# Kernel optimization log

Hardware: AMD Instinct MI355X
Metric: run time of the kernel (lower is better)

## Reference

```python
import jax, jax.numpy as jnp
import numpy as np
from jax import lax

V, H, A, S = 256, 2048, 512, 512  # vocab, hidden, attn, seq_len


def setup_inputs() -> dict:
    key = jax.random.key(0)
    ks = jax.random.split(key, 8)
    sc = 0.02  # small init to keep tanh unsaturated
    return {
        "x_enc": jax.random.normal(ks[0], (S, V), jnp.float32),
        "x_dec": jax.random.normal(ks[1], (S, V), jnp.float32),
        "W_enc": jax.random.normal(ks[2], (H, V + H), jnp.float32) * sc,
        "b_enc": jnp.zeros((H,), jnp.float32),
        "Wa_enc": jax.random.normal(ks[3], (A, H), jnp.float32) * sc,
        "Wa_dec": jax.random.normal(ks[4], (A, H), jnp.float32) * sc,
        "v_a": jax.random.normal(ks[5], (A,), jnp.float32) * sc,
        "W_dec": jax.random.normal(ks[6], (H, V + 2 * H), jnp.float32) * sc,
        "b_dec": jnp.zeros((H,), jnp.float32),
        "W_out": jax.random.normal(ks[7], (V, H), jnp.float32) * sc,
        "b_out": jnp.zeros((V,), jnp.float32),
    }


def reference(x_enc, x_dec, W_enc, b_enc, Wa_enc, Wa_dec, v_a, W_dec, b_dec, W_out, b_out):
    h0 = jnp.zeros((W_enc.shape[0],), x_enc.dtype)

    # Encoder: h_t = tanh(W_enc [x_t ; h_{t-1}] + b)
    def enc_step(h, x):
        h_new = jnp.tanh(jnp.concatenate([x, h]) @ W_enc.T + b_enc)
        return h_new, h_new

    h_enc, enc_states = lax.scan(enc_step, h0, x_enc)  # enc_states: (S, H)

    # Encoder-side attention projection is step-invariant -> hoist (same math).
    enc_proj = enc_states @ Wa_enc.T  # (S, A)

    # Decoder with per-step Bahdanau additive attention.
    def dec_step(h, x):
        dec_proj = h @ Wa_dec.T                              # (A,)
        energy = jnp.tanh(enc_proj + dec_proj) @ v_a         # (S,)
        attn_w = jax.nn.softmax(energy)                      # (S,)
        context = attn_w @ enc_states                        # (H,)
        h_new = jnp.tanh(jnp.concatenate([x, context, h]) @ W_dec.T + b_dec)
        logits = h_new @ W_out.T + b_out                     # (V,)
        return h_new, logits

    _, outputs = lax.scan(dec_step, h_enc, x_dec)  # (S, V)
    return outputs
```

## Files before the change

### kernel.cpp

```cpp
#include <hip/hip_runtime.h>

#define V 256
#define H 2048
#define A 512
#define S 512
#define NBLK 128
#define NTHR 512
#define CH 64
#define HPH (512*CH)
#define DPH (128*CH)
#define SENTU 0x7FC00000u

typedef float f32x4 __attribute__((ext_vector_type(4)));
typedef float f32x2 __attribute__((ext_vector_type(2)));

__device__ __forceinline__ f32x4 ld_cg4(const float* p) {
    f32x4 r;
    asm volatile("global_load_dwordx4 %0, %1, off sc0 sc1\n\ts_waitcnt vmcnt(0)"
                 : "=&v"(r) : "v"(p) : "memory");
    return r;
}
__device__ __forceinline__ f32x4 poll4(const float* p) {
    f32x4 r = ld_cg4(p);
    while (__float_as_uint(r.x) == SENTU || __float_as_uint(r.y) == SENTU ||
           __float_as_uint(r.z) == SENTU || __float_as_uint(r.w) == SENTU)
        r = ld_cg4(p);
    return r;
}
__device__ __forceinline__ void st_pub2(float* p, float x, float y) {
    f32x2 v; v.x = x; v.y = y;
    asm volatile("s_waitcnt vmcnt(0)\n\tglobal_store_dwordx2 %0, %1, off sc0 sc1"
                 :: "v"(p), "v"(v) : "memory");
}
__device__ __forceinline__ void st_pub1(float* p, float x) {
    asm volatile("s_waitcnt vmcnt(0)\n\tglobal_store_dword %0, %1, off sc0 sc1"
                 :: "v"(p), "v"(x) : "memory");
}
__device__ __forceinline__ void st_rst2(float* p) {
    f32x2 v; v.x = __uint_as_float(SENTU); v.y = __uint_as_float(SENTU);
    asm volatile("global_store_dwordx2 %0, %1, off sc0 sc1" :: "v"(p), "v"(v) : "memory");
}
__device__ __forceinline__ void st_rst1(float* p) {
    float v = __uint_as_float(SENTU);
    asm volatile("global_store_dword %0, %1, off sc0 sc1" :: "v"(p), "v"(v) : "memory");
}

__global__ void init_ex(unsigned* p, int n) {
    int i = blockIdx.x * blockDim.x + threadIdx.x;
    if (i < n) p[i] = SENTU;
}

__global__ __launch_bounds__(256) void gemm_nt(
    const float* __restrict__ Amat, int lda,
    const float* __restrict__ Bmat, int ldb,
    float* __restrict__ C, int ldc,
    const float* __restrict__ bias, int M, int N, int K)
{
    __shared__ float As[16][68];
    __shared__ float Bs[16][68];
    const int tid = threadIdx.x;
    const int tx = tid & 15;
    const int ty = tid >> 4;
    const int m0 = blockIdx.y * 64;
    const int n0 = blockIdx.x * 64;
    const int lr = tid >> 2;
    const int lk = (tid & 3) * 4;

    float acc[4][4] = {};
    for (int k0 = 0; k0 < K; k0 += 16) {
        float4 av = *(const float4*)(Amat + (size_t)(m0 + lr) * lda + k0 + lk);
        float4 bv = *(const float4*)(Bmat + (size_t)(n0 + lr) * ldb + k0 + lk);
        __syncthreads();
        As[lk+0][lr] = av.x; As[lk+1][lr] = av.y; As[lk+2][lr] = av.z; As[lk+3][lr] = av.w;
        Bs[lk+0][lr] = bv.x; Bs[lk+1][lr] = bv.y; Bs[lk+2][lr] = bv.z; Bs[lk+3][lr] = bv.w;
        __syncthreads();
        #pragma unroll
        for (int k = 0; k < 16; ++k) {
            float a4[4], b4[4];
            #pragma unroll
            for (int i = 0; i < 4; ++i) a4[i] = As[k][ty*4+i];
            #pragma unroll
            for (int j = 0; j < 4; ++j) b4[j] = Bs[k][tx*4+j];
            #pragma unroll
            for (int i = 0; i < 4; ++i)
                #pragma unroll
                for (int j = 0; j < 4; ++j) acc[i][j] += a4[i] * b4[j];
        }
    }
    #pragma unroll
    for (int i = 0; i < 4; ++i) {
        const int m = m0 + ty*4 + i;
        #pragma unroll
        for (int j = 0; j < 4; ++j) {
            const int n = n0 + tx*4 + j;
            float v = acc[i][j];
            if (bias) v += bias[n];
            C[(size_t)m * ldc + n] = v;
        }
    }
}

__global__ __launch_bounds__(NTHR, 2) void enc_scan(
    const float* __restrict__ W_enc, const float* __restrict__ accx,
    float* __restrict__ states, float* __restrict__ hex)
{
    __shared__ __align__(16) float hs[2][H];
    const int tid = threadIdx.x;
    const int wid = tid >> 6, lane = tid & 63;
    const int w   = blockIdx.x * 8 + wid;
    const int r0  = 2*w, r1 = r0 + 1;
    const int slot = (w >> 1)*CH + (w & 1)*2;

    f32x4 we0[8], we1[8];
    #pragma unroll
    for (int k = 0; k < 8; ++k) {
        we0[k] = *(const f32x4*)(W_enc + (size_t)r0*(V+H) + V + 4*(lane + 64*k));
        we1[k] = *(const f32x4*)(W_enc + (size_t)r1*(V+H) + V + 4*(lane + 64*k));
    }

    if (lane == 0) {
        float h0 = tanhf(accx[r0]), h1 = tanhf(accx[r1]);
        states[r0] = h0; states[r1] = h1;
        st_pub2(hex + slot, h0, h1);
    }

    for (int t = 1; t < S; ++t) {
        float ax0 = 0.f, ax1 = 0.f;
        if (lane == 0) { ax0 = accx[(size_t)t*H + r0]; ax1 = accx[(size_t)t*H + r1]; }

        f32x4 c = poll4(hex + ((t-1)%3)*HPH + tid*CH);
        ((f32x4*)hs[t&1])[tid] = c;
        __syncthreads();

        if (lane == 0) st_rst2(hex + ((t+1)%3)*HPH + slot);

        const f32x4* h4 = (const f32x4*)hs[t&1];
        float a0 = 0.f, a1 = 0.f;
        #pragma unroll
        for (int k = 0; k < 8; ++k) {
            f32x4 hv = h4[lane + 64*k];
            a0 += we0[k].x*hv.x + we0[k].y*hv.y + we0[k].z*hv.z + we0[k].w*hv.w;
            a1 += we1[k].x*hv.x + we1[k].y*hv.y + we1[k].z*hv.z + we1[k].w*hv.w;
        }
        #pragma unroll
        for (int off = 32; off; off >>= 1) { a0 += __shfl_down(a0, off); a1 += __shfl_down(a1, off); }
        if (lane == 0) {
            float h0 = tanhf(a0 + ax0);
            float h1 = tanhf(a1 + ax1);
            states[(size_t)t*H + r0] = h0; states[(size_t)t*H + r1] = h1;
            st_pub2(hex + (t%3)*HPH + slot, h0, h1);
        }
    }
}

__global__ __launch_bounds__(NTHR, 2) void dec_scan(
    const float* __restrict__ Wa_dec, const float* __restrict__ W_dec,
    const float* __restrict__ enc_proj, const float* __restrict__ v_a,
    const float* __restrict__ WcT, const float* __restrict__ accx,
    const float* __restrict__ enc_states, float* __restrict__ h_dec,
    float* __restrict__ hexd, float* __restrict__ dpex, float* __restrict__ eex)
{
    __shared__ __align__(16) float hs[H];
    __shared__ __align__(16) float ps[A];
    __shared__ __align__(16) float es[S];
    __shared__ float zred[8];
    const int tid = threadIdx.x;
    const int wid = tid >> 6, lane = tid & 63;
    const int w   = blockIdx.x * 8 + wid;
    const int r0  = 2*w, r1 = r0 + 1;
    const int hslot = (w >> 1)*CH + (w & 1)*2;
    const bool attn = ((w & 1) == 0);
    const int s_row = w >> 1;
    const int aslot = (s_row >> 2)*CH + (s_row & 3);

    f32x4 wh0[8], wh1[8], wa[8], wc0[2], wc1[2], ep[2], va[2];
    #pragma unroll
    for (int k = 0; k < 8; ++k) {
        wh0[k] = *(const f32x4*)(W_dec + (size_t)r0*(V+2*H) + V + H + 4*(lane + 64*k));
        wh1[k] = *(const f32x4*)(W_dec + (size_t)r1*(V+2*H) + V + H + 4*(lane + 64*k));
        wa[k]  = (f32x4)(0.f);
    }
    #pragma unroll
    for (int k = 0; k < 2; ++k) {
        wc0[k] = *(const f32x4*)(WcT + (size_t)r0*S + 4*(lane + 64*k));
        wc1[k] = *(const f32x4*)(WcT + (size_t)r1*S + 4*(lane + 64*k));
        ep[k] = (f32x4)(0.f); va[k] = (f32x4)(0.f);
    }
    if (attn) {
        #pragma unroll
        for (int k = 0; k < 8; ++k)
            wa[k] = *(const f32x4*)(Wa_dec + (size_t)s_row*H + 4*(lane + 64*k));
        #pragma unroll
        for (int k = 0; k < 2; ++k) {
            ep[k] = *(const f32x4*)(enc_proj + (size_t)s_row*A + 4*(lane + 64*k));
            va[k] = *(const f32x4*)(v_a + 4*(lane + 64*k));
        }
    }
    const f32x4* hs4 = (const f32x4*)hs;
    const f32x4* ps4 = (const f32x4*)ps;
    const f32x4* es4 = (const f32x4*)es;

    for (int t = 0; t < S; ++t) {
        float ax0 = 0.f, ax1 = 0.f;
        if (lane == 0) { ax0 = accx[(size_t)t*H + r0]; ax1 = accx[(size_t)t*H + r1]; }

        if (t == 0) {
            ((f32x4*)hs)[tid] = ((const f32x4*)(enc_states + (size_t)(S-1)*H))[tid];
        } else {
            f32x4 c = poll4(hexd + ((t-1)%3)*HPH + tid*CH);
            ((f32x4*)hs)[tid] = c;
        }
        __syncthreads();

        if (t > 0 && lane == 0) {
            st_rst2(hexd + ((t+1)%3)*HPH + hslot);
            if (attn) {
                st_rst1(dpex + ((t-1)%3)*DPH + aslot);
                st_rst1(eex  + ((t-1)%3)*DPH + aslot);
            }
        }

        if (attn) {
            float aP = 0.f;
            #pragma unroll
            for (int k = 0; k < 8; ++k) {
                f32x4 hv = hs4[lane + 64*k];
                aP += wa[k].x*hv.x + wa[k].y*hv.y + wa[k].z*hv.z + wa[k].w*hv.w;
            }
            #pragma unroll
            for (int off = 32; off; off >>= 1) aP += __shfl_down(aP, off);
            if (lane == 0) st_pub1(dpex + (t%3)*DPH + aslot, aP);
        }
        float aH0 = 0.f, aH1 = 0.f;
        #pragma unroll
        for (int k = 0; k < 8; ++k) {
            f32x4 hv = hs4[lane + 64*k];
            aH0 += wh0[k].x*hv.x + wh0[k].y*hv.y + wh0[k].z*hv.z + wh0[k].w*hv.w;
            aH1 += wh1[k].x*hv.x + wh1[k].y*hv.y + wh1[k].z*hv.z + wh1[k].w*hv.w;
        }
        #pragma unroll
        for (int off = 32; off; off >>= 1) { aH0 += __shfl_down(aH0, off); aH1 += __shfl_down(aH1, off); }

        if (tid < 128) {
            f32x4 c = poll4(dpex + (t%3)*DPH + tid*CH);
            ((f32x4*)ps)[tid] = c;
        }
        __syncthreads();
        if (attn) {
            float e_ = 0.f;
            #pragma unroll
            for (int k = 0; k < 2; ++k) {
                f32x4 p = ps4[lane + 64*k];
                e_ += va[k].x*tanhf(ep[k].x + p.x) + va[k].y*tanhf(ep[k].y + p.y)
                    + va[k].z*tanhf(ep[k].z + p.z) + va[k].w*tanhf(ep[k].w + p.w);
            }
            #pragma unroll
            for (int off = 32; off; off >>= 1) e_ += __shfl_down(e_, off);
            if (lane == 0) st_pub1(eex + (t%3)*DPH + aslot, expf(e_));
        }

        if (tid < 128) {
            f32x4 c = poll4(eex + (t%3)*DPH + tid*CH);
            ((f32x4*)es)[tid] = c;
        }
        __syncthreads();

        float z = es[tid];
        #pragma unroll
        for (int off = 32; off; off >>= 1) z += __shfl_down(z, off);
        if (lane == 0) zred[wid] = z;
        __syncthreads();
        const float Z = zred[0]+zred[1]+zred[2]+zred[3]+zred[4]+zred[5]+zred[6]+zred[7];

        float c0 = 0.f, c1 = 0.f;
        #pragma unroll
        for (int k = 0; k < 2; ++k) {
            f32x4 ev = es4[lane + 64*k];
            c0 += wc0[k].x*ev.x + wc0[k].y*ev.y + wc0[k].z*ev.z + wc0[k].w*ev.w;
            c1 += wc1[k].x*ev.x + wc1[k].y*ev.y + wc1[k].z*ev.z + wc1[k].w*ev.w;
        }
        #pragma unroll
        for (int off = 32; off; off >>= 1) { c0 += __shfl_down(c0, off); c1 += __shfl_down(c1, off); }
        if (lane == 0) {
            const float Zi = 1.f / Z;
            float h0 = tanhf(ax0 + aH0 + c0*Zi);
            float h1 = tanhf(ax1 + aH1 + c1*Zi);
            h_dec[(size_t)t*H + r0] = h0; h_dec[(size_t)t*H + r1] = h1;
            st_pub2(hexd + (t%3)*HPH + hslot, h0, h1);
        }
    }
}

extern "C" void kernel_launch(void* const* d_in, const int* in_sizes, int n_in,
                              void* d_out, int out_size, void* d_ws, size_t ws_size,
                              hipStream_t stream) {
    const float* x_enc  = (const float*)d_in[0];
    const float* x_dec  = (const float*)d_in[1];
    const float* W_enc  = (const float*)d_in[2];
    const float* b_enc  = (const float*)d_in[3];
    const float* Wa_enc = (const float*)d_in[4];
    const float* Wa_dec = (const float*)d_in[5];
    const float* v_a    = (const float*)d_in[6];
    const float* W_dec  = (const float*)d_in[7];
    const float* b_dec  = (const float*)d_in[8];
    const float* W_out  = (const float*)d_in[9];
    const float* b_out  = (const float*)d_in[10];
    float* out = (float*)d_out;

    float* ws         = (float*)d_ws;
    float* accx_enc   = ws;
    float* enc_states = accx_enc + (size_t)S*H;
    float* enc_proj   = enc_states + (size_t)S*H;
    float* WcT        = enc_proj + (size_t)S*A;
    float* accx_dec   = WcT + (size_t)H*S;
    float* h_dec      = accx_dec + (size_t)S*H;
    float* hex_e      = h_dec + (size_t)S*H;
    float* hex_d      = hex_e + 3*HPH;
    float* dp_ex      = hex_d + 3*HPH;
    float* e_ex       = dp_ex + 3*DPH;
    const int n_ex = 3*HPH*2 + 3*DPH*2;

    dim3 b256(256);

    init_ex<<<dim3((n_ex + 255)/256), b256, 0, stream>>>((unsigned*)hex_e, n_ex);

    gemm_nt<<<dim3(H/64, S/64), b256, 0, stream>>>(x_enc, V, W_enc, V+H, accx_enc, H, b_enc, S, H, V);
    gemm_nt<<<dim3(H/64, S/64), b256, 0, stream>>>(x_dec, V, W_dec, V+2*H, accx_dec, H, b_dec, S, H, V);

    {
        const float* We = W_enc; const float* ax = accx_enc; float* st = enc_states; float* hx = hex_e;
        void* args[] = { &We, &ax, &st, &hx };
        hipLaunchCooperativeKernel((void*)enc_scan, dim3(NBLK), dim3(NTHR), args, 0, stream);
    }

    gemm_nt<<<dim3(A/64, S/64), b256, 0, stream>>>(enc_states, H, Wa_enc, H, enc_proj, A, nullptr, S, A, H);
    gemm_nt<<<dim3(S/64, H/64), b256, 0, stream>>>(W_dec + V, V+2*H, enc_states, H, WcT, S, nullptr, H, S, H);

    {
        const float* wa = Wa_dec; const float* wd = W_dec; const float* epj = enc_proj;
        const float* vv = v_a; const float* wc = WcT; const float* ax = accx_dec;
        const float* est = enc_states; float* hd = h_dec;
        float* hx = hex_d; float* dx = dp_ex; float* ex = e_ex;
        void* args[] = { &wa, &wd, &epj, &vv, &wc, &ax, &est, &hd, &hx, &dx, &ex };
        hipLaunchCooperativeKernel((void*)dec_scan, dim3(NBLK), dim3(NTHR), args, 0, stream);
    }

    gemm_nt<<<dim3(V/64, S/64), b256, 0, stream>>>(h_dec, H, W_out, H, out, V, b_out, S, V, H);
}
```

Baseline: 6.185 ms.

## Replace packed vector-load polling with per-producer atomic slots

Cross-block exchange buffers are re-laid out so that each producing wave owns its own 256-byte slot. Values are published and polled with device-scope relaxed atomic exchange and fetch_add instead of sc0/sc1 vector loads and stores into shared 16-byte groups. This is meant to cut false sharing and repeated polling of cache lines that several producers write. The cost is more poll operations per thread (two 64-bit polls for h, one poll per thread for attention values instead of 128 threads) and atomics that travel to L2.

```diff
diff --git a/kernel.cpp b/kernel.cpp
--- a/kernel.cpp
+++ b/kernel.cpp
@@ -7,42 +7,32 @@
 #define NBLK 128
 #define NTHR 512
 #define CH 64
-#define HPH (512*CH)
-#define DPH (128*CH)
+#define HPH (1024*CH)
+#define DPH (512*CH)
 #define SENTU 0x7FC00000u
+#define SENT64 0x7FC000007FC00000ULL
 
 typedef float f32x4 __attribute__((ext_vector_type(4)));
-typedef float f32x2 __attribute__((ext_vector_type(2)));
-
-__device__ __forceinline__ f32x4 ld_cg4(const float* p) {
-    f32x4 r;
-    asm volatile("global_load_dwordx4 %0, %1, off sc0 sc1\n\ts_waitcnt vmcnt(0)"
-                 : "=&v"(r) : "v"(p) : "memory");
-    return r;
-}
-__device__ __forceinline__ f32x4 poll4(const float* p) {
-    f32x4 r = ld_cg4(p);
-    while (__float_as_uint(r.x) == SENTU || __float_as_uint(r.y) == SENTU ||
-           __float_as_uint(r.z) == SENTU || __float_as_uint(r.w) == SENTU)
-        r = ld_cg4(p);
-    return r;
-}
-__device__ __forceinline__ void st_pub2(float* p, float x, float y) {
-    f32x2 v; v.x = x; v.y = y;
-    asm volatile("s_waitcnt vmcnt(0)\n\tglobal_store_dwordx2 %0, %1, off sc0 sc1"
-                 :: "v"(p), "v"(v) : "memory");
-}
-__device__ __forceinline__ void st_pub1(float* p, float x) {
-    asm volatile("s_waitcnt vmcnt(0)\n\tglobal_store_dword %0, %1, off sc0 sc1"
-                 :: "v"(p), "v"(x) : "memory");
-}
-__device__ __forceinline__ void st_rst2(float* p) {
-    f32x2 v; v.x = __uint_as_float(SENTU); v.y = __uint_as_float(SENTU);
-    asm volatile("global_store_dwordx2 %0, %1, off sc0 sc1" :: "v"(p), "v"(v) : "memory");
-}
-__device__ __forceinline__ void st_rst1(float* p) {
-    float v = __uint_as_float(SENTU);
-    asm volatile("global_store_dword %0, %1, off sc0 sc1" :: "v"(p), "v"(v) : "memory");
+typedef unsigned long long u64;
+
+__device__ __forceinline__ void vm_drain() { asm volatile("s_waitcnt vmcnt(0)" ::: "memory"); }
+__device__ __forceinline__ u64 ax_poll64(u64* p) {
+    return __hip_atomic_fetch_add(p, 0ULL, __ATOMIC_RELAXED, __HIP_MEMORY_SCOPE_AGENT);
+}
+__device__ __forceinline__ unsigned ax_poll32(unsigned* p) {
+    return __hip_atomic_fetch_add(p, 0u, __ATOMIC_RELAXED, __HIP_MEMORY_SCOPE_AGENT);
+}
+__device__ __forceinline__ void ax_st64(u64* p, u64 v) {
+    (void)__hip_atomic_exchange(p, v, __ATOMIC_RELAXED, __HIP_MEMORY_SCOPE_AGENT);
+}
+__device__ __forceinline__ void ax_st32(unsigned* p, unsigned v) {
+    (void)__hip_atomic_exchange(p, v, __ATOMIC_RELAXED, __HIP_MEMORY_SCOPE_AGENT);
+}
+__device__ __forceinline__ bool bad64(u64 v) {
+    return ((unsigned)v == SENTU) || ((unsigned)(v >> 32) == SENTU);
+}
+__device__ __forceinline__ u64 pack2(float a, float b) {
+    return ((u64)__float_as_uint(b) << 32) | (u64)__float_as_uint(a);
 }
 
 __global__ void init_ex(unsigned* p, int n) {
@@ -109,7 +99,6 @@
     const int wid = tid >> 6, lane = tid & 63;
     const int w   = blockIdx.x * 8 + wid;
     const int r0  = 2*w, r1 = r0 + 1;
-    const int slot = (w >> 1)*CH + (w & 1)*2;
 
     f32x4 we0[8], we1[8];
     #pragma unroll
@@ -121,18 +110,30 @@
     if (lane == 0) {
         float h0 = tanhf(accx[r0]), h1 = tanhf(accx[r1]);
         states[r0] = h0; states[r1] = h1;
-        st_pub2(hex + slot, h0, h1);
+        vm_drain();
+        ax_st64((u64*)(hex + 0*HPH + w*CH), pack2(h0, h1));
     }
 
     for (int t = 1; t < S; ++t) {
         float ax0 = 0.f, ax1 = 0.f;
         if (lane == 0) { ax0 = accx[(size_t)t*H + r0]; ax1 = accx[(size_t)t*H + r1]; }
 
-        f32x4 c = poll4(hex + ((t-1)%3)*HPH + tid*CH);
-        ((f32x4*)hs[t&1])[tid] = c;
-        __syncthreads();
-
-        if (lane == 0) st_rst2(hex + ((t+1)%3)*HPH + slot);
+        {
+            float* hb = hex + ((t-1)%3)*HPH;
+            u64* s0 = (u64*)(hb + tid*CH);
+            u64* s1 = (u64*)(hb + (tid+512)*CH);
+            u64 a = ax_poll64(s0), b = ax_poll64(s1);
+            while (bad64(a)) a = ax_poll64(s0);
+            while (bad64(b)) b = ax_poll64(s1);
+            float* dst = hs[t&1];
+            dst[2*tid]        = __uint_as_float((unsigned)a);
+            dst[2*tid+1]      = __uint_as_float((unsigned)(a >> 32));
+            dst[1024+2*tid]   = __uint_as_float((unsigned)b);
+            dst[1024+2*tid+1] = __uint_as_float((unsigned)(b >> 32));
+        }
+        __syncthreads();
+
+        if (lane == 0) ax_st64((u64*)(hex + ((t+1)%3)*HPH + w*CH), SENT64);
 
         const f32x4* h4 = (const f32x4*)hs[t&1];
         float a0 = 0.f, a1 = 0.f;
@@ -148,7 +149,8 @@
             float h0 = tanhf(a0 + ax0);
             float h1 = tanhf(a1 + ax1);
             states[(size_t)t*H + r0] = h0; states[(size_t)t*H + r1] = h1;
-            st_pub2(hex + (t%3)*HPH + slot, h0, h1);
+            vm_drain();
+            ax_st64((u64*)(hex + (t%3)*HPH + w*CH), pack2(h0, h1));
         }
     }
 }
@@ -168,10 +170,8 @@
     const int wid = tid >> 6, lane = tid & 63;
     const int w   = blockIdx.x * 8 + wid;
     const int r0  = 2*w, r1 = r0 + 1;
-    const int hslot = (w >> 1)*CH + (w & 1)*2;
     const bool attn = ((w & 1) == 0);
     const int s_row = w >> 1;
-    const int aslot = (s_row >> 2)*CH + (s_row & 3);
 
     f32x4 wh0[8], wh1[8], wa[8], wc0[2], wc1[2], ep[2], va[2];
     #pragma unroll
@@ -207,16 +207,24 @@
         if (t == 0) {
             ((f32x4*)hs)[tid] = ((const f32x4*)(enc_states + (size_t)(S-1)*H))[tid];
         } else {
-            f32x4 c = poll4(hexd + ((t-1)%3)*HPH + tid*CH);
-            ((f32x4*)hs)[tid] = c;
+            float* hb = hexd + ((t-1)%3)*HPH;
+            u64* s0 = (u64*)(hb + tid*CH);
+            u64* s1 = (u64*)(hb + (tid+512)*CH);
+            u64 a = ax_poll64(s0), b = ax_poll64(s1);
+            while (bad64(a)) a = ax_poll64(s0);
+            while (bad64(b)) b = ax_poll64(s1);
+            hs[2*tid]        = __uint_as_float((unsigned)a);
+            hs[2*tid+1]      = __uint_as_float((unsigned)(a >> 32));
+            hs[1024+2*tid]   = __uint_as_float((unsigned)b);
+            hs[1024+2*tid+1] = __uint_as_float((unsigned)(b >> 32));
         }
         __syncthreads();
 
         if (t > 0 && lane == 0) {
-            st_rst2(hexd + ((t+1)%3)*HPH + hslot);
+            ax_st64((u64*)(hexd + ((t+1)%3)*HPH + w*CH), SENT64);
             if (attn) {
-                st_rst1(dpex + ((t-1)%3)*DPH + aslot);
-                st_rst1(eex  + ((t-1)%3)*DPH + aslot);
+                ax_st32((unsigned*)(dpex + ((t-1)%3)*DPH + s_row*CH), SENTU);
+                ax_st32((unsigned*)(eex  + ((t-1)%3)*DPH + s_row*CH), SENTU);
             }
         }
 
@@ -229,7 +237,10 @@
             }
             #pragma unroll
             for (int off = 32; off; off >>= 1) aP += __shfl_down(aP, off);
-            if (lane == 0) st_pub1(dpex + (t%3)*DPH + aslot, aP);
+            if (lane == 0) {
+                vm_drain();
+                ax_st32((unsigned*)(dpex + (t%3)*DPH + s_row*CH), __float_as_uint(aP));
+            }
         }
         float aH0 = 0.f, aH1 = 0.f;
         #pragma unroll
@@ -241,9 +252,11 @@
         #pragma unroll
         for (int off = 32; off; off >>= 1) { aH0 += __shfl_down(aH0, off); aH1 += __shfl_down(aH1, off); }
 
-        if (tid < 128) {
-            f32x4 c = poll4(dpex + (t%3)*DPH + tid*CH);
-            ((f32x4*)ps)[tid] = c;
+        {
+            unsigned* sp = (unsigned*)(dpex + (t%3)*DPH + tid*CH);
+            unsigned v = ax_poll32(sp);
+            while (v == SENTU) v = ax_poll32(sp);
+            ps[tid] = __uint_as_float(v);
         }
         __syncthreads();
         if (attn) {
@@ -256,12 +269,17 @@
             }
             #pragma unroll
             for (int off = 32; off; off >>= 1) e_ += __shfl_down(e_, off);
-            if (lane == 0) st_pub1(eex + (t%3)*DPH + aslot, expf(e_));
-        }
-
-        if (tid < 128) {
-            f32x4 c = poll4(eex + (t%3)*DPH + tid*CH);
-            ((f32x4*)es)[tid] = c;
+            if (lane == 0) {
+                vm_drain();
+                ax_st32((unsigned*)(eex + (t%3)*DPH + s_row*CH), __float_as_uint(expf(e_)));
+            }
+        }
+
+        {
+            unsigned* sp = (unsigned*)(eex + (t%3)*DPH + tid*CH);
+            unsigned v = ax_poll32(sp);
+            while (v == SENTU) v = ax_poll32(sp);
+            es[tid] = __uint_as_float(v);
         }
         __syncthreads();
 
@@ -286,7 +304,8 @@
             float h0 = tanhf(ax0 + aH0 + c0*Zi);
             float h1 = tanhf(ax1 + aH1 + c1*Zi);
             h_dec[(size_t)t*H + r0] = h0; h_dec[(size_t)t*H + r1] = h1;
-            st_pub2(hexd + (t%3)*HPH + hslot, h0, h1);
+            vm_drain();
+            ax_st64((u64*)(hexd + (t%3)*HPH + w*CH), pack2(h0, h1));
         }
     }
 }
```

Measured after the change: 6.156 ms. About the same (-0.5%).

## Compute next-step decoder attention projection via atomic scatter, cutting one grid exchange

Applied to the files above, without the earlier changes.

In the decoder scan, each block now computes its partial contribution to the next step's Wa_dec·h projection from the h values it just produced. It accumulates these into a global buffer with float atomics and signals completion through a counter. A separate kernel computes the step-0 projection. This removes one full cross-block publish/poll round (the dp exchange) from each step's critical path, and the encoder and decoder now publish via atomic exchanges while resetting sentinels in the same step. The cost is many global float atomics per step, a counter spin-wait, a different floating-point summation order, and occupancy lowered to one block per CU.

```diff
diff --git a/kernel.cpp b/kernel.cpp
--- a/kernel.cpp
+++ b/kernel.cpp
@@ -7,12 +7,16 @@
 #define NBLK 128
 #define NTHR 512
 #define CH 64
+#define CH2 16
 #define HPH (512*CH)
-#define DPH (128*CH)
+#define EPH (128*CH)
+#define DPH (512*CH2)
 #define SENTU 0x7FC00000u
+#define SENT64 0x7FC000007FC00000ULL
 
 typedef float f32x4 __attribute__((ext_vector_type(4)));
 typedef float f32x2 __attribute__((ext_vector_type(2)));
+typedef unsigned long long u64;
 
 __device__ __forceinline__ f32x4 ld_cg4(const float* p) {
     f32x4 r;
@@ -27,27 +31,54 @@
         r = ld_cg4(p);
     return r;
 }
-__device__ __forceinline__ void st_pub2(float* p, float x, float y) {
-    f32x2 v; v.x = x; v.y = y;
-    asm volatile("s_waitcnt vmcnt(0)\n\tglobal_store_dwordx2 %0, %1, off sc0 sc1"
-                 :: "v"(p), "v"(v) : "memory");
-}
-__device__ __forceinline__ void st_pub1(float* p, float x) {
-    asm volatile("s_waitcnt vmcnt(0)\n\tglobal_store_dword %0, %1, off sc0 sc1"
-                 :: "v"(p), "v"(x) : "memory");
-}
-__device__ __forceinline__ void st_rst2(float* p) {
-    f32x2 v; v.x = __uint_as_float(SENTU); v.y = __uint_as_float(SENTU);
-    asm volatile("global_store_dwordx2 %0, %1, off sc0 sc1" :: "v"(p), "v"(v) : "memory");
-}
-__device__ __forceinline__ void st_rst1(float* p) {
-    float v = __uint_as_float(SENTU);
-    asm volatile("global_store_dword %0, %1, off sc0 sc1" :: "v"(p), "v"(v) : "memory");
-}
-
-__global__ void init_ex(unsigned* p, int n) {
+__device__ __forceinline__ unsigned ld_cg1u(const unsigned* p) {
+    unsigned r;
+    asm volatile("global_load_dword %0, %1, off sc0 sc1\n\ts_waitcnt vmcnt(0)"
+                 : "=&v"(r) : "v"(p) : "memory");
+    return r;
+}
+__device__ __forceinline__ void ld_cg8(const float* p0, const float* p1, const float* p2, const float* p3,
+                                       const float* p4, const float* p5, const float* p6, const float* p7,
+                                       float o[8]) {
+    float a0,a1,a2,a3,a4,a5,a6,a7;
+    asm volatile(
+        "global_load_dword %0, %8, off sc0 sc1\n\t"
+        "global_load_dword %1, %9, off sc0 sc1\n\t"
+        "global_load_dword %2, %10, off sc0 sc1\n\t"
+        "global_load_dword %3, %11, off sc0 sc1\n\t"
+        "global_load_dword %4, %12, off sc0 sc1\n\t"
+        "global_load_dword %5, %13, off sc0 sc1\n\t"
+        "global_load_dword %6, %14, off sc0 sc1\n\t"
+        "global_load_dword %7, %15, off sc0 sc1\n\t"
+        "s_waitcnt vmcnt(0)"
+        : "=&v"(a0),"=&v"(a1),"=&v"(a2),"=&v"(a3),"=&v"(a4),"=&v"(a5),"=&v"(a6),"=&v"(a7)
+        : "v"(p0),"v"(p1),"v"(p2),"v"(p3),"v"(p4),"v"(p5),"v"(p6),"v"(p7)
+        : "memory");
+    o[0]=a0;o[1]=a1;o[2]=a2;o[3]=a3;o[4]=a4;o[5]=a5;o[6]=a6;o[7]=a7;
+}
+
+__device__ __forceinline__ void vm_drain() { asm volatile("s_waitcnt vmcnt(0)" ::: "memory"); }
+__device__ __forceinline__ void ax_st64(u64* p, u64 v) {
+    (void)__hip_atomic_exchange(p, v, __ATOMIC_RELAXED, __HIP_MEMORY_SCOPE_AGENT);
+}
+__device__ __forceinline__ void ax_st32(unsigned* p, unsigned v) {
+    (void)__hip_atomic_exchange(p, v, __ATOMIC_RELAXED, __HIP_MEMORY_SCOPE_AGENT);
+}
+__device__ __forceinline__ float ga_addf(float* p, float v) {
+    return __hip_atomic_fetch_add(p, v, __ATOMIC_RELAXED, __HIP_MEMORY_SCOPE_AGENT);
+}
+__device__ __forceinline__ unsigned ga_addu(unsigned* p, unsigned v) {
+    return __hip_atomic_fetch_add(p, v, __ATOMIC_RELAXED, __HIP_MEMORY_SCOPE_AGENT);
+}
+__device__ __forceinline__ u64 pack2(float a, float b) {
+    return ((u64)__float_as_uint(b) << 32) | (u64)__float_as_uint(a);
+}
+
+__global__ void init_ex(unsigned* sent, int n_sent, unsigned* zero, int n_zero, unsigned* cnt) {
     int i = blockIdx.x * blockDim.x + threadIdx.x;
-    if (i < n) p[i] = SENTU;
+    if (i < n_sent) sent[i] = SENTU;
+    if (i < n_zero) zero[i] = 0u;
+    if (i == 0) { cnt[0] = NBLK; cnt[64] = 0u; cnt[128] = 0u; }
 }
 
 __global__ __launch_bounds__(256) void gemm_nt(
@@ -100,11 +131,30 @@
     }
 }
 
+__global__ __launch_bounds__(512) void dp0_kernel(
+    const float* __restrict__ Wa_dec, const float* __restrict__ hN, float* __restrict__ dpacc)
+{
+    const int wid = threadIdx.x >> 6, lane = threadIdx.x & 63;
+    const int a   = blockIdx.x * 8 + wid;
+    const f32x4* w4 = (const f32x4*)(Wa_dec + (size_t)a * H);
+    const f32x4* h4 = (const f32x4*)hN;
+    float acc = 0.f;
+    #pragma unroll
+    for (int k = 0; k < 8; ++k) {
+        f32x4 w = w4[lane + 64*k];
+        f32x4 h = h4[lane + 64*k];
+        acc += w.x*h.x + w.y*h.y + w.z*h.z + w.w*h.w;
+    }
+    #pragma unroll
+    for (int off = 32; off; off >>= 1) acc += __shfl_down(acc, off);
+    if (lane == 0) ax_st32((unsigned*)(dpacc + (size_t)a*CH2), __float_as_uint(acc));
+}
+
 __global__ __launch_bounds__(NTHR, 2) void enc_scan(
     const float* __restrict__ W_enc, const float* __restrict__ accx,
     float* __restrict__ states, float* __restrict__ hex)
 {
-    __shared__ __align__(16) float hs[2][H];
+    __shared__ __align__(16) float hs[H];
     const int tid = threadIdx.x;
     const int wid = tid >> 6, lane = tid & 63;
     const int w   = blockIdx.x * 8 + wid;
@@ -120,21 +170,18 @@
 
     if (lane == 0) {
         float h0 = tanhf(accx[r0]), h1 = tanhf(accx[r1]);
+        vm_drain();
+        ax_st64((u64*)(hex + 0*HPH + slot), pack2(h0, h1));
         states[r0] = h0; states[r1] = h1;
-        st_pub2(hex + slot, h0, h1);
     }
 
     for (int t = 1; t < S; ++t) {
-        float ax0 = 0.f, ax1 = 0.f;
-        if (lane == 0) { ax0 = accx[(size_t)t*H + r0]; ax1 = accx[(size_t)t*H + r1]; }
-
-        f32x4 c = poll4(hex + ((t-1)%3)*HPH + tid*CH);
-        ((f32x4*)hs[t&1])[tid] = c;
-        __syncthreads();
-
-        if (lane == 0) st_rst2(hex + ((t+1)%3)*HPH + slot);
-
-        const f32x4* h4 = (const f32x4*)hs[t&1];
+        float ax0 = accx[(size_t)t*H + r0];
+        float ax1 = accx[(size_t)t*H + r1];
+        ((f32x4*)hs)[tid] = poll4(hex + ((t-1)%3)*HPH + tid*CH);
+        __syncthreads();
+
+        const f32x4* h4 = (const f32x4*)hs;
         float a0 = 0.f, a1 = 0.f;
         #pragma unroll
         for (int k = 0; k < 8; ++k) {
@@ -147,90 +194,93 @@
         if (lane == 0) {
             float h0 = tanhf(a0 + ax0);
             float h1 = tanhf(a1 + ax1);
+            vm_drain();
+            ax_st64((u64*)(hex + (t%3)*HPH + slot), pack2(h0, h1));
             states[(size_t)t*H + r0] = h0; states[(size_t)t*H + r1] = h1;
-            st_pub2(hex + (t%3)*HPH + slot, h0, h1);
-        }
-    }
-}
-
-__global__ __launch_bounds__(NTHR, 2) void dec_scan(
+            ax_st64((u64*)(hex + ((t+1)%3)*HPH + slot), SENT64);
+        }
+    }
+}
+
+__global__ __launch_bounds__(NTHR, 1) void dec_scan(
     const float* __restrict__ Wa_dec, const float* __restrict__ W_dec,
     const float* __restrict__ enc_proj, const float* __restrict__ v_a,
     const float* __restrict__ WcT, const float* __restrict__ accx,
     const float* __restrict__ enc_states, float* __restrict__ h_dec,
-    float* __restrict__ hexd, float* __restrict__ dpex, float* __restrict__ eex)
+    float* __restrict__ hexd, float* __restrict__ eex,
+    float* __restrict__ dpacc, unsigned* __restrict__ cnt)
 {
     __shared__ __align__(16) float hs[H];
-    __shared__ __align__(16) float ps[A];
     __shared__ __align__(16) float es[S];
+    __shared__ float dpl[A];
     __shared__ float zred[8];
     const int tid = threadIdx.x;
     const int wid = tid >> 6, lane = tid & 63;
-    const int w   = blockIdx.x * 8 + wid;
+    const int bid = blockIdx.x;
+    const int w   = bid * 8 + wid;
     const int r0  = 2*w, r1 = r0 + 1;
     const int hslot = (w >> 1)*CH + (w & 1)*2;
     const bool attn = ((w & 1) == 0);
     const int s_row = w >> 1;
-    const int aslot = (s_row >> 2)*CH + (s_row & 3);
-
-    f32x4 wh0[8], wh1[8], wa[8], wc0[2], wc1[2], ep[2], va[2];
+
+    f32x4 wh0[8], wh1[8], wc0[2], wc1[2];
+    float ep_r[8], va_r[8], wac0[8], wac1[8];
     #pragma unroll
     for (int k = 0; k < 8; ++k) {
         wh0[k] = *(const f32x4*)(W_dec + (size_t)r0*(V+2*H) + V + H + 4*(lane + 64*k));
         wh1[k] = *(const f32x4*)(W_dec + (size_t)r1*(V+2*H) + V + H + 4*(lane + 64*k));
-        wa[k]  = (f32x4)(0.f);
+        wac0[k] = Wa_dec[(size_t)(lane + 64*k)*H + r0];
+        wac1[k] = Wa_dec[(size_t)(lane + 64*k)*H + r1];
+        ep_r[k] = 0.f; va_r[k] = 0.f;
     }
     #pragma unroll
     for (int k = 0; k < 2; ++k) {
         wc0[k] = *(const f32x4*)(WcT + (size_t)r0*S + 4*(lane + 64*k));
         wc1[k] = *(const f32x4*)(WcT + (size_t)r1*S + 4*(lane + 64*k));
-        ep[k] = (f32x4)(0.f); va[k] = (f32x4)(0.f);
     }
     if (attn) {
         #pragma unroll
-        for (int k = 0; k < 8; ++k)
-            wa[k] = *(const f32x4*)(Wa_dec + (size_t)s_row*H + 4*(lane + 64*k));
-        #pragma unroll
-        for (int k = 0; k < 2; ++k) {
-            ep[k] = *(const f32x4*)(enc_proj + (size_t)s_row*A + 4*(lane + 64*k));
-            va[k] = *(const f32x4*)(v_a + 4*(lane + 64*k));
+        for (int k = 0; k < 8; ++k) {
+            ep_r[k] = enc_proj[(size_t)s_row*A + lane + 64*k];
+            va_r[k] = v_a[lane + 64*k];
         }
     }
     const f32x4* hs4 = (const f32x4*)hs;
-    const f32x4* ps4 = (const f32x4*)ps;
     const f32x4* es4 = (const f32x4*)es;
 
     for (int t = 0; t < S; ++t) {
-        float ax0 = 0.f, ax1 = 0.f;
-        if (lane == 0) { ax0 = accx[(size_t)t*H + r0]; ax1 = accx[(size_t)t*H + r1]; }
-
-        if (t == 0) {
-            ((f32x4*)hs)[tid] = ((const f32x4*)(enc_states + (size_t)(S-1)*H))[tid];
-        } else {
-            f32x4 c = poll4(hexd + ((t-1)%3)*HPH + tid*CH);
-            ((f32x4*)hs)[tid] = c;
-        }
-        __syncthreads();
-
-        if (t > 0 && lane == 0) {
-            st_rst2(hexd + ((t+1)%3)*HPH + hslot);
-            if (attn) {
-                st_rst1(dpex + ((t-1)%3)*DPH + aslot);
-                st_rst1(eex  + ((t-1)%3)*DPH + aslot);
-            }
-        }
+        const int ph  = t % 3;
+        const int phn = (t+1) % 3;
+        const int php = (t+2) % 3;
+
+        if (t == 0) ((f32x4*)hs)[tid] = ((const f32x4*)(enc_states + (size_t)(S-1)*H))[tid];
+        else        ((f32x4*)hs)[tid] = poll4(hexd + php*HPH + tid*CH);
+        __syncthreads();
 
         if (attn) {
-            float aP = 0.f;
-            #pragma unroll
-            for (int k = 0; k < 8; ++k) {
-                f32x4 hv = hs4[lane + 64*k];
-                aP += wa[k].x*hv.x + wa[k].y*hv.y + wa[k].z*hv.z + wa[k].w*hv.w;
-            }
-            #pragma unroll
-            for (int off = 32; off; off >>= 1) aP += __shfl_down(aP, off);
-            if (lane == 0) st_pub1(dpex + (t%3)*DPH + aslot, aP);
-        }
+            float* dpb = dpacc + ph*DPH;
+            const float* q0 = dpb + (size_t)(lane      )*CH2;
+            const float* q1 = dpb + (size_t)(lane +  64)*CH2;
+            const float* q2 = dpb + (size_t)(lane + 128)*CH2;
+            const float* q3 = dpb + (size_t)(lane + 192)*CH2;
+            const float* q4 = dpb + (size_t)(lane + 256)*CH2;
+            const float* q5 = dpb + (size_t)(lane + 320)*CH2;
+            const float* q6 = dpb + (size_t)(lane + 384)*CH2;
+            const float* q7 = dpb + (size_t)(lane + 448)*CH2;
+            const unsigned* cp = cnt + ph*64;
+            while (ld_cg1u(cp) < NBLK) {}
+            float dpv[8];
+            ld_cg8(q0,q1,q2,q3,q4,q5,q6,q7, dpv);
+            float e_ = 0.f;
+            #pragma unroll
+            for (int k = 0; k < 8; ++k) e_ += va_r[k] * tanhf(ep_r[k] + dpv[k]);
+            #pragma unroll
+            for (int off = 32; off; off >>= 1) e_ += __shfl_xor(e_, off);
+            if (lane == 0)
+                ax_st32((unsigned*)(eex + ph*EPH + (s_row>>2)*CH + (s_row&3)),
+                        __float_as_uint(expf(e_)));
+        }
+
         float aH0 = 0.f, aH1 = 0.f;
         #pragma unroll
         for (int k = 0; k < 8; ++k) {
@@ -239,35 +289,14 @@
             aH1 += wh1[k].x*hv.x + wh1[k].y*hv.y + wh1[k].z*hv.z + wh1[k].w*hv.w;
         }
         #pragma unroll
-        for (int off = 32; off; off >>= 1) { aH0 += __shfl_down(aH0, off); aH1 += __shfl_down(aH1, off); }
-
-        if (tid < 128) {
-            f32x4 c = poll4(dpex + (t%3)*DPH + tid*CH);
-            ((f32x4*)ps)[tid] = c;
-        }
-        __syncthreads();
-        if (attn) {
-            float e_ = 0.f;
-            #pragma unroll
-            for (int k = 0; k < 2; ++k) {
-                f32x4 p = ps4[lane + 64*k];
-                e_ += va[k].x*tanhf(ep[k].x + p.x) + va[k].y*tanhf(ep[k].y + p.y)
-                    + va[k].z*tanhf(ep[k].z + p.z) + va[k].w*tanhf(ep[k].w + p.w);
-            }
-            #pragma unroll
-            for (int off = 32; off; off >>= 1) e_ += __shfl_down(e_, off);
-            if (lane == 0) st_pub1(eex + (t%3)*DPH + aslot, expf(e_));
-        }
-
-        if (tid < 128) {
-            f32x4 c = poll4(eex + (t%3)*DPH + tid*CH);
-            ((f32x4*)es)[tid] = c;
-        }
+        for (int off = 32; off; off >>= 1) { aH0 += __shfl_xor(aH0, off); aH1 += __shfl_xor(aH1, off); }
+
+        if (tid < 128) ((f32x4*)es)[tid] = poll4(eex + ph*EPH + tid*CH);
         __syncthreads();
 
         float z = es[tid];
         #pragma unroll
-        for (int off = 32; off; off >>= 1) z += __shfl_down(z, off);
+        for (int off = 32; off; off >>= 1) z += __shfl_xor(z, off);
         if (lane == 0) zred[wid] = z;
         __syncthreads();
         const float Z = zred[0]+zred[1]+zred[2]+zred[3]+zred[4]+zred[5]+zred[6]+zred[7];
@@ -280,14 +309,38 @@
             c1 += wc1[k].x*ev.x + wc1[k].y*ev.y + wc1[k].z*ev.z + wc1[k].w*ev.w;
         }
         #pragma unroll
-        for (int off = 32; off; off >>= 1) { c0 += __shfl_down(c0, off); c1 += __shfl_down(c1, off); }
+        for (int off = 32; off; off >>= 1) { c0 += __shfl_xor(c0, off); c1 += __shfl_xor(c1, off); }
+
+        const float Zi = 1.f / Z;
+        const float ax0 = accx[(size_t)t*H + r0];
+        const float ax1 = accx[(size_t)t*H + r1];
+        const float h0 = tanhf(ax0 + aH0 + c0*Zi);
+        const float h1 = tanhf(ax1 + aH1 + c1*Zi);
         if (lane == 0) {
-            const float Zi = 1.f / Z;
-            float h0 = tanhf(ax0 + aH0 + c0*Zi);
-            float h1 = tanhf(ax1 + aH1 + c1*Zi);
-            h_dec[(size_t)t*H + r0] = h0; h_dec[(size_t)t*H + r1] = h1;
-            st_pub2(hexd + (t%3)*HPH + hslot, h0, h1);
-        }
+            vm_drain();
+            ax_st64((u64*)(hexd + ph*HPH + hslot), pack2(h0, h1));
+            f32x2 hv; hv.x = h0; hv.y = h1;
+            *(f32x2*)(h_dec + (size_t)t*H + r0) = hv;
+        }
+
+        if (t < S-1) {
+            dpl[tid] = 0.f;
+            __syncthreads();
+            #pragma unroll
+            for (int k = 0; k < 8; ++k)
+                atomicAdd(&dpl[lane + 64*k], wac0[k]*h0 + wac1[k]*h1);
+            __syncthreads();
+            (void)ga_addf(dpacc + phn*DPH + (size_t)tid*CH2, dpl[tid]);
+            vm_drain();
+            __syncthreads();
+            if (tid == 0) (void)ga_addu(cnt + phn*64, 1u);
+        }
+
+        if (lane == 0) ax_st64((u64*)(hexd + phn*HPH + hslot), SENT64);
+        if (t > 0 && attn && lane == 0)
+            ax_st32((unsigned*)(eex + php*EPH + (s_row>>2)*CH + (s_row&3)), SENTU);
+        if (tid < 4) ax_st32((unsigned*)(dpacc + ph*DPH + (size_t)(4*bid+tid)*CH2), 0u);
+        if (bid == 0 && tid == 0) ax_st32(cnt + ph*64, 0u);
     }
 }
 
@@ -316,13 +369,16 @@
     float* h_dec      = accx_dec + (size_t)S*H;
     float* hex_e      = h_dec + (size_t)S*H;
     float* hex_d      = hex_e + 3*HPH;
-    float* dp_ex      = hex_d + 3*HPH;
-    float* e_ex       = dp_ex + 3*DPH;
-    const int n_ex = 3*HPH*2 + 3*DPH*2;
+    float* e_ex       = hex_d + 3*HPH;
+    float* dpacc      = e_ex + 3*EPH;
+    unsigned* cnt     = (unsigned*)(dpacc + 3*DPH);
+    const int n_sent = 3*HPH*2 + 3*EPH;
+    const int n_zero = 3*DPH;
 
     dim3 b256(256);
 
-    init_ex<<<dim3((n_ex + 255)/256), b256, 0, stream>>>((unsigned*)hex_e, n_ex);
+    init_ex<<<dim3((n_sent + 255)/256), b256, 0, stream>>>(
+        (unsigned*)hex_e, n_sent, (unsigned*)dpacc, n_zero, cnt);
 
     gemm_nt<<<dim3(H/64, S/64), b256, 0, stream>>>(x_enc, V, W_enc, V+H, accx_enc, H, b_enc, S, H, V);
     gemm_nt<<<dim3(H/64, S/64), b256, 0, stream>>>(x_dec, V, W_dec, V+2*H, accx_dec, H, b_dec, S, H, V);
@@ -335,13 +391,16 @@
 
     gemm_nt<<<dim3(A/64, S/64), b256, 0, stream>>>(enc_states, H, Wa_enc, H, enc_proj, A, nullptr, S, A, H);
     gemm_nt<<<dim3(S/64, H/64), b256, 0, stream>>>(W_dec + V, V+2*H, enc_states, H, WcT, S, nullptr, H, S, H);
+    {
+        dp0_kernel<<<dim3(64), dim3(512), 0, stream>>>(Wa_dec, enc_states + (size_t)(S-1)*H, dpacc);
+    }
 
     {
         const float* wa = Wa_dec; const float* wd = W_dec; const float* epj = enc_proj;
         const float* vv = v_a; const float* wc = WcT; const float* ax = accx_dec;
         const float* est = enc_states; float* hd = h_dec;
-        float* hx = hex_d; float* dx = dp_ex; float* ex = e_ex;
-        void* args[] = { &wa, &wd, &epj, &vv, &wc, &ax, &est, &hd, &hx, &dx, &ex };
+        float* hx = hex_d; float* ex = e_ex; float* dpa = dpacc; unsigned* cc = cnt;
+        void* args[] = { &wa, &wd, &epj, &vv, &wc, &ax, &est, &hd, &hx, &ex, &dpa, &cc };
         hipLaunchCooperativeKernel((void*)dec_scan, dim3(NBLK), dim3(NTHR), args, 0, stream);
     }
 
```

Result: slower. 10.35 ms (+67.3%).

## Aggregate per-block hidden-state publishes into 64-byte chunks for cross-block exchange

Applied to the files above, without the earlier changes.

Each block now gathers its 16 hidden outputs in shared memory and one thread publishes them as a single 64-byte chunk per block, instead of each wave publishing a 2-float slot into a padded 64-float line. Readers poll 128 chunks with four 16-byte loads each rather than 512 padded slots, which shrinks the exchange buffer and the number of coherent global transactions per step. The cost is an extra __syncthreads before each publish, and a single publisher thread per block on the serial critical path. It also drops the double-buffered shared hidden array in the encoder.

```diff
diff --git a/kernel.cpp b/kernel.cpp
--- a/kernel.cpp
+++ b/kernel.cpp
@@ -7,7 +7,7 @@
 #define NBLK 128
 #define NTHR 512
 #define CH 64
-#define HPH (512*CH)
+#define HPH (128*CH)
 #define DPH (128*CH)
 #define SENTU 0x7FC00000u
 
@@ -27,18 +27,39 @@
         r = ld_cg4(p);
     return r;
 }
-__device__ __forceinline__ void st_pub2(float* p, float x, float y) {
-    f32x2 v; v.x = x; v.y = y;
-    asm volatile("s_waitcnt vmcnt(0)\n\tglobal_store_dwordx2 %0, %1, off sc0 sc1"
-                 :: "v"(p), "v"(v) : "memory");
+__device__ __forceinline__ void ld_cg16(const float* p, f32x4& a, f32x4& b, f32x4& c, f32x4& d) {
+    asm volatile("global_load_dwordx4 %0, %4, off sc0 sc1\n\t"
+                 "global_load_dwordx4 %1, %5, off sc0 sc1\n\t"
+                 "global_load_dwordx4 %2, %6, off sc0 sc1\n\t"
+                 "global_load_dwordx4 %3, %7, off sc0 sc1\n\t"
+                 "s_waitcnt vmcnt(0)"
+                 : "=&v"(a), "=&v"(b), "=&v"(c), "=&v"(d)
+                 : "v"(p), "v"(p+4), "v"(p+8), "v"(p+12) : "memory");
+}
+__device__ __forceinline__ bool anynan(f32x4 v) {
+    return __float_as_uint(v.x) == SENTU || __float_as_uint(v.y) == SENTU ||
+           __float_as_uint(v.z) == SENTU || __float_as_uint(v.w) == SENTU;
+}
+__device__ __forceinline__ void st_pub16(float* p, f32x4 a, f32x4 b, f32x4 c, f32x4 d) {
+    asm volatile("s_waitcnt vmcnt(0)\n\t"
+                 "global_store_dwordx4 %0, %4, off sc0 sc1\n\t"
+                 "global_store_dwordx4 %1, %5, off sc0 sc1\n\t"
+                 "global_store_dwordx4 %2, %6, off sc0 sc1\n\t"
+                 "global_store_dwordx4 %3, %7, off sc0 sc1"
+                 :: "v"(p), "v"(p+4), "v"(p+8), "v"(p+12),
+                    "v"(a), "v"(b), "v"(c), "v"(d) : "memory");
+}
+__device__ __forceinline__ void st_rst16(float* p) {
+    f32x4 s; s.x = s.y = s.z = s.w = __uint_as_float(SENTU);
+    asm volatile("global_store_dwordx4 %0, %4, off sc0 sc1\n\t"
+                 "global_store_dwordx4 %1, %4, off sc0 sc1\n\t"
+                 "global_store_dwordx4 %2, %4, off sc0 sc1\n\t"
+                 "global_store_dwordx4 %3, %4, off sc0 sc1"
+                 :: "v"(p), "v"(p+4), "v"(p+8), "v"(p+12), "v"(s) : "memory");
 }
 __device__ __forceinline__ void st_pub1(float* p, float x) {
     asm volatile("s_waitcnt vmcnt(0)\n\tglobal_store_dword %0, %1, off sc0 sc1"
                  :: "v"(p), "v"(x) : "memory");
-}
-__device__ __forceinline__ void st_rst2(float* p) {
-    f32x2 v; v.x = __uint_as_float(SENTU); v.y = __uint_as_float(SENTU);
-    asm volatile("global_store_dwordx2 %0, %1, off sc0 sc1" :: "v"(p), "v"(v) : "memory");
 }
 __device__ __forceinline__ void st_rst1(float* p) {
     float v = __uint_as_float(SENTU);
@@ -104,12 +125,13 @@
     const float* __restrict__ W_enc, const float* __restrict__ accx,
     float* __restrict__ states, float* __restrict__ hex)
 {
-    __shared__ __align__(16) float hs[2][H];
+    __shared__ __align__(16) float hs[H];
+    __shared__ __align__(16) float hout[16];
     const int tid = threadIdx.x;
     const int wid = tid >> 6, lane = tid & 63;
-    const int w   = blockIdx.x * 8 + wid;
+    const int bid = blockIdx.x;
+    const int w   = bid * 8 + wid;
     const int r0  = 2*w, r1 = r0 + 1;
-    const int slot = (w >> 1)*CH + (w & 1)*2;
 
     f32x4 we0[8], we1[8];
     #pragma unroll
@@ -118,23 +140,31 @@
         we1[k] = *(const f32x4*)(W_enc + (size_t)r1*(V+H) + V + 4*(lane + 64*k));
     }
 
-    if (lane == 0) {
+    {
         float h0 = tanhf(accx[r0]), h1 = tanhf(accx[r1]);
-        states[r0] = h0; states[r1] = h1;
-        st_pub2(hex + slot, h0, h1);
+        if (lane == 0) { hout[2*wid] = h0; hout[2*wid+1] = h1; }
+        __syncthreads();
+        if (tid == 0) {
+            const f32x4* g = (const f32x4*)hout;
+            st_pub16(hex + 0*HPH + bid*CH, g[0], g[1], g[2], g[3]);
+        }
+        if (lane == 0) { states[r0] = h0; states[r1] = h1; }
     }
 
     for (int t = 1; t < S; ++t) {
-        float ax0 = 0.f, ax1 = 0.f;
-        if (lane == 0) { ax0 = accx[(size_t)t*H + r0]; ax1 = accx[(size_t)t*H + r1]; }
-
-        f32x4 c = poll4(hex + ((t-1)%3)*HPH + tid*CH);
-        ((f32x4*)hs[t&1])[tid] = c;
-        __syncthreads();
-
-        if (lane == 0) st_rst2(hex + ((t+1)%3)*HPH + slot);
-
-        const f32x4* h4 = (const f32x4*)hs[t&1];
+        float ax0 = accx[(size_t)t*H + r0];
+        float ax1 = accx[(size_t)t*H + r1];
+        if (tid < 128) {
+            const float* cp = hex + ((t-1)%3)*HPH + tid*CH;
+            f32x4 a, b, c, d;
+            do { ld_cg16(cp, a, b, c, d); } while (anynan(a)||anynan(b)||anynan(c)||anynan(d));
+            f32x4* dst = (f32x4*)(hs + 16*tid);
+            dst[0] = a; dst[1] = b; dst[2] = c; dst[3] = d;
+        }
+        __syncthreads();
+        if (tid == 0) st_rst16(hex + ((t+1)%3)*HPH + bid*CH);
+
+        const f32x4* h4 = (const f32x4*)hs;
         float a0 = 0.f, a1 = 0.f;
         #pragma unroll
         for (int k = 0; k < 8; ++k) {
@@ -144,11 +174,18 @@
         }
         #pragma unroll
         for (int off = 32; off; off >>= 1) { a0 += __shfl_down(a0, off); a1 += __shfl_down(a1, off); }
+        float h0 = 0.f, h1 = 0.f;
         if (lane == 0) {
-            float h0 = tanhf(a0 + ax0);
-            float h1 = tanhf(a1 + ax1);
+            h0 = tanhf(a0 + ax0); h1 = tanhf(a1 + ax1);
+            hout[2*wid] = h0; hout[2*wid+1] = h1;
+        }
+        __syncthreads();
+        if (tid == 0) {
+            const f32x4* g = (const f32x4*)hout;
+            st_pub16(hex + (t%3)*HPH + bid*CH, g[0], g[1], g[2], g[3]);
+        }
+        if (lane == 0) {
             states[(size_t)t*H + r0] = h0; states[(size_t)t*H + r1] = h1;
-            st_pub2(hex + (t%3)*HPH + slot, h0, h1);
         }
     }
 }
@@ -163,12 +200,13 @@
     __shared__ __align__(16) float hs[H];
     __shared__ __align__(16) float ps[A];
     __shared__ __align__(16) float es[S];
+    __shared__ __align__(16) float hout[16];
     __shared__ float zred[8];
     const int tid = threadIdx.x;
     const int wid = tid >> 6, lane = tid & 63;
-    const int w   = blockIdx.x * 8 + wid;
+    const int bid = blockIdx.x;
+    const int w   = bid * 8 + wid;
     const int r0  = 2*w, r1 = r0 + 1;
-    const int hslot = (w >> 1)*CH + (w & 1)*2;
     const bool attn = ((w & 1) == 0);
     const int s_row = w >> 1;
     const int aslot = (s_row >> 2)*CH + (s_row & 3);
@@ -201,23 +239,28 @@
     const f32x4* es4 = (const f32x4*)es;
 
     for (int t = 0; t < S; ++t) {
-        float ax0 = 0.f, ax1 = 0.f;
-        if (lane == 0) { ax0 = accx[(size_t)t*H + r0]; ax1 = accx[(size_t)t*H + r1]; }
+        const int ph  = t % 3;
+        const int phn = (t+1) % 3;
+        const int php = (t+2) % 3;
+
+        float ax0 = accx[(size_t)t*H + r0];
+        float ax1 = accx[(size_t)t*H + r1];
 
         if (t == 0) {
             ((f32x4*)hs)[tid] = ((const f32x4*)(enc_states + (size_t)(S-1)*H))[tid];
-        } else {
-            f32x4 c = poll4(hexd + ((t-1)%3)*HPH + tid*CH);
-            ((f32x4*)hs)[tid] = c;
-        }
-        __syncthreads();
-
-        if (t > 0 && lane == 0) {
-            st_rst2(hexd + ((t+1)%3)*HPH + hslot);
-            if (attn) {
-                st_rst1(dpex + ((t-1)%3)*DPH + aslot);
-                st_rst1(eex  + ((t-1)%3)*DPH + aslot);
-            }
+        } else if (tid < 128) {
+            const float* cp = hexd + php*HPH + tid*CH;
+            f32x4 a, b, c, d;
+            do { ld_cg16(cp, a, b, c, d); } while (anynan(a)||anynan(b)||anynan(c)||anynan(d));
+            f32x4* dst = (f32x4*)(hs + 16*tid);
+            dst[0] = a; dst[1] = b; dst[2] = c; dst[3] = d;
+        }
+        __syncthreads();
+
+        if (tid == 0) st_rst16(hexd + phn*HPH + bid*CH);
+        if (t > 0 && attn && lane == 0) {
+            st_rst1(dpex + php*DPH + aslot);
+            st_rst1(eex  + php*DPH + aslot);
         }
 
         if (attn) {
@@ -229,7 +272,7 @@
             }
             #pragma unroll
             for (int off = 32; off; off >>= 1) aP += __shfl_down(aP, off);
-            if (lane == 0) st_pub1(dpex + (t%3)*DPH + aslot, aP);
+            if (lane == 0) st_pub1(dpex + ph*DPH + aslot, aP);
         }
         float aH0 = 0.f, aH1 = 0.f;
         #pragma unroll
@@ -241,10 +284,7 @@
         #pragma unroll
         for (int off = 32; off; off >>= 1) { aH0 += __shfl_down(aH0, off); aH1 += __shfl_down(aH1, off); }
 
-        if (tid < 128) {
-            f32x4 c = poll4(dpex + (t%3)*DPH + tid*CH);
-            ((f32x4*)ps)[tid] = c;
-        }
+        if (tid < 128) ((f32x4*)ps)[tid] = poll4(dpex + ph*DPH + tid*CH);
         __syncthreads();
         if (attn) {
             float e_ = 0.f;
@@ -256,13 +296,10 @@
             }
             #pragma unroll
             for (int off = 32; off; off >>= 1) e_ += __shfl_down(e_, off);
-            if (lane == 0) st_pub1(eex + (t%3)*DPH + aslot, expf(e_));
-        }
-
-        if (tid < 128) {
-            f32x4 c = poll4(eex + (t%3)*DPH + tid*CH);
-            ((f32x4*)es)[tid] = c;
-        }
+            if (lane == 0) st_pub1(eex + ph*DPH + aslot, expf(e_));
+        }
+
+        if (tid < 128) ((f32x4*)es)[tid] = poll4(eex + ph*DPH + tid*CH);
         __syncthreads();
 
         float z = es[tid];
@@ -281,12 +318,22 @@
         }
         #pragma unroll
         for (int off = 32; off; off >>= 1) { c0 += __shfl_down(c0, off); c1 += __shfl_down(c1, off); }
+
+        float h0 = 0.f, h1 = 0.f;
         if (lane == 0) {
             const float Zi = 1.f / Z;
-            float h0 = tanhf(ax0 + aH0 + c0*Zi);
-            float h1 = tanhf(ax1 + aH1 + c1*Zi);
-            h_dec[(size_t)t*H + r0] = h0; h_dec[(size_t)t*H + r1] = h1;
-            st_pub2(hexd + (t%3)*HPH + hslot, h0, h1);
+            h0 = tanhf(ax0 + aH0 + c0*Zi);
+            h1 = tanhf(ax1 + aH1 + c1*Zi);
+            hout[2*wid] = h0; hout[2*wid+1] = h1;
+        }
+        __syncthreads();
+        if (tid == 0) {
+            const f32x4* g = (const f32x4*)hout;
+            st_pub16(hexd + ph*HPH + bid*CH, g[0], g[1], g[2], g[3]);
+        }
+        if (lane == 0) {
+            f32x2 hv; hv.x = h0; hv.y = h1;
+            *(f32x2*)(h_dec + (size_t)t*H + r0) = hv;
         }
     }
 }
```

Result: slower. 6.383 ms (+3.2%).
